# Kernel tuning notes

Hardware: AMD Instinct MI355X
Metric: run time of the kernel (lower is better)

The kernel has to match this reference:

```python
import jax, jax.numpy as jnp
import numpy as np

B, T, C, H = 2, 2048, 2048, 16
HD = C // H


def setup_inputs() -> dict:
    key = jax.random.key(0)
    ks = jax.random.split(key, 5)
    s = 0.02  # init scale for weights
    return {
        "x": jax.random.normal(ks[0], (B, T, C), jnp.float32),
        "Wq": jax.random.normal(ks[1], (C, C), jnp.float32) * s,
        "Wk": jax.random.normal(ks[2], (C, C), jnp.float32) * s,
        "Wv": jax.random.normal(ks[3], (C, C), jnp.float32) * s,
        "Wo": jax.random.normal(ks[4], (C, C), jnp.float32) * s,
        "bo": jnp.zeros((C,), jnp.float32),
    }


def _alibi_slopes(n_head):
    # power-of-2 path of _get_alibi_slopes (n_head=16 is a power of 2)
    return jnp.array([1.0 / 2 ** (i + 1) for i in range(n_head)], jnp.float32)


def reference(x, Wq, Wk, Wv, Wo, bo):
    b, t, c = x.shape
    h, hd = H, HD
    scale = 1.0 / np.sqrt(hd)
    # nn.Linear (no bias): y = x @ W.T; split heads -> (B,H,T,HD)
    q = (x @ Wq.T).reshape(b, t, h, hd).transpose(0, 2, 1, 3)
    k = (x @ Wk.T).reshape(b, t, h, hd).transpose(0, 2, 1, 3)
    v = (x @ Wv.T).reshape(b, t, h, hd).transpose(0, 2, 1, 3)
    scores = jnp.einsum("bhtd,bhsd->bhts", q, k) * scale  # (B,H,T,T)
    pos = jnp.arange(t)
    diff = pos[:, None] - pos[None, :]  # (T,T), i-j
    slopes = _alibi_slopes(h)
    bias = slopes[:, None, None] * diff.astype(jnp.float32)  # (H,T,T)
    causal = diff >= 0  # lower-triangular mask
    bias = jnp.where(causal[None, :, :], bias, -jnp.inf)
    scores = scores + bias[None]  # (B,H,T,T)
    attn = jax.nn.softmax(scores, axis=-1)  # dropout = identity (eval mode)
    out = jnp.einsum("bhts,bhsd->bhtd", attn, v)
    out = out.transpose(0, 2, 1, 3).reshape(b, t, c)
    out = out @ Wo.T + bo  # proj_dropout = identity (eval mode)
    return out, attn
```

## Files before the change

### kernel.cpp

```cpp
#include <hip/hip_runtime.h>
#include <hip/hip_bf16.h>

#define DEVINL __device__ __forceinline__

typedef __attribute__((ext_vector_type(8))) short bf16x8;
typedef __attribute__((ext_vector_type(4))) float f32x4;

DEVINL ushort f2bf(float f) {
  unsigned u = __float_as_uint(f);
  u += 0x7fffu + ((u >> 16) & 1u);
  return (ushort)(u >> 16);
}

DEVINL void gl_lds16(const void* g, void* lds) {
  __builtin_amdgcn_global_load_lds(
      (const __attribute__((address_space(1))) void*)g,
      (__attribute__((address_space(3))) void*)lds, 16, 0, 0);
}

DEVINL f32x4 mfma16(bf16x8 a, bf16x8 b, f32x4 c) {
  return __builtin_amdgcn_mfma_f32_16x16x32_bf16(a, b, c, 0, 0, 0);
}

__global__ __launch_bounds__(256) void cast_bf16_kernel(const float4* __restrict__ in,
                                                        ushort4* __restrict__ out, int n4) {
  int stride = (int)(gridDim.x * blockDim.x);
  for (int i = (int)(blockIdx.x * blockDim.x + threadIdx.x); i < n4; i += stride) {
    float4 v = in[i];
    out[i] = make_ushort4(f2bf(v.x), f2bf(v.y), f2bf(v.z), f2bf(v.w));
  }
}

template <int OUTMODE>
__global__ __launch_bounds__(256) void gemm_nt(const ushort* __restrict__ A,
                                               const ushort* __restrict__ Bm,
                                               void* __restrict__ Cout,
                                               const float* __restrict__ bias,
                                               int M, int N, int K) {
  __shared__ __align__(16) ushort Al[8192];
  __shared__ __align__(16) ushort Bl[8192];
  const int tid = (int)threadIdx.x;
  const int l = tid & 63, w = tid >> 6;
  const int wr = w >> 1, wc = w & 1;
  const int lr = l & 15, lg = l >> 4;
  const int rowT = (int)blockIdx.y * 128, colT = (int)blockIdx.x * 128;

  f32x4 acc[4][4] = {};

  for (int kt = 0; kt < K; kt += 64) {
#pragma unroll
    for (int q = 0; q < 4; ++q) {
      int s = q * 256 + tid;
      int rb = s >> 7, ks = (s >> 6) & 1, sl = s & 63;
      size_t koff = (size_t)(kt + ks * 32 + (sl >> 4) * 8);
      gl_lds16(A + (size_t)(rowT + rb * 16 + (sl & 15)) * K + koff,
               Al + (size_t)(q * 256 + (tid & 192)) * 8);
      gl_lds16(Bm + (size_t)(colT + rb * 16 + (sl & 15)) * K + koff,
               Bl + (size_t)(q * 256 + (tid & 192)) * 8);
    }
    __syncthreads();
#pragma unroll
    for (int ks = 0; ks < 2; ++ks) {
      bf16x8 af[4], bfv[4];
#pragma unroll
      for (int i = 0; i < 4; ++i) {
        af[i]  = *(const bf16x8*)(Al + (((wr * 4 + i) * 2 + ks) * 64 + l) * 8);
        bfv[i] = *(const bf16x8*)(Bl + (((wc * 4 + i) * 2 + ks) * 64 + l) * 8);
      }
#pragma unroll
      for (int i = 0; i < 4; ++i)
#pragma unroll
        for (int j = 0; j < 4; ++j)
          acc[i][j] = mfma16(af[i], bfv[j], acc[i][j]);
    }
    __syncthreads();
  }

#pragma unroll
  for (int i = 0; i < 4; ++i) {
#pragma unroll
    for (int j = 0; j < 4; ++j) {
      const int col = colT + wc * 64 + j * 16 + lr;
#pragma unroll
      for (int e = 0; e < 4; ++e) {
        const int row = rowT + wr * 64 + i * 16 + lg * 4 + e;
        float v = acc[i][j][e];
        if (OUTMODE == 0) {
          ((ushort*)Cout)[(size_t)row * N + col] = f2bf(v);
        } else if (OUTMODE == 1) {
          ((ushort*)Cout)[((size_t)((row >> 11) * 2048 + col)) * 2048 + (row & 2047)] = f2bf(v);
        } else {
          ((float*)Cout)[(size_t)row * N + col] = v + bias[col];
        }
      }
    }
  }
}

__global__ __launch_bounds__(256) void flash_kernel(const ushort* __restrict__ Qg,
                                                    const ushort* __restrict__ Kg,
                                                    const ushort* __restrict__ Vt,
                                                    ushort* __restrict__ Og,
                                                    float2* __restrict__ stats) {
  __shared__ __align__(16) ushort Kl[2][8192];
  __shared__ __align__(16) ushort Vl[2][8192];
  __shared__ __align__(16) ushort Pl[4][1024];

  const int flat = (int)(blockIdx.y * gridDim.x + blockIdx.x);
  const int swz = (flat & 7) * 64 + (flat >> 3);
  const int bx = swz & 15, bh = swz >> 4;
  const int b = bh >> 4, h = bh & 15;
  const int tid = (int)threadIdx.x, l = tid & 63, w = tid >> 6;
  const int lr = l & 15, lg = l >> 4;
  const float scale = 0.08838834764831845f;
  const float slope = exp2f(-(float)(h + 1));
  const ushort* Kbase = Kg + ((size_t)b * 2048) * 2048 + h * 128;
  const ushort* Vbase = Vt + ((size_t)b * 2048 + h * 128) * 2048;

  for (int half = 0; half < 2; ++half) {
    const int qb = (half == 0) ? 31 - bx : bx;
    const int qr0 = qb * 64 + w * 16;

    bf16x8 qf[4];
#pragma unroll
    for (int ks = 0; ks < 4; ++ks)
      qf[ks] = *(const bf16x8*)(Qg + ((size_t)b * 2048 + qr0 + lr) * 2048 + h * 128 + ks * 32 + lg * 8);

    float runmax[4], runsum[4];
    f32x4 o[8] = {};
#pragma unroll
    for (int j = 0; j < 4; ++j) { runmax[j] = -__builtin_inff(); runsum[j] = 0.f; }

    auto stage = [&](int jt, int buf) {
#pragma unroll
      for (int q = 0; q < 4; ++q) {
        const int s = q * 256 + tid;
        const int sl = s & 63;
        const int cb = s >> 8, ks = (s >> 6) & 3;
        gl_lds16(Kbase + (size_t)(jt * 64 + cb * 16 + (sl & 15)) * 2048 + ks * 32 + (sl >> 4) * 8,
                 &Kl[buf][(size_t)(q * 256 + (tid & 192)) * 8]);
        const int db = s >> 7, k2 = (s >> 6) & 1;
        gl_lds16(Vbase + (size_t)(db * 16 + (sl & 15)) * 2048 + jt * 64 + k2 * 32 + (sl >> 4) * 8,
                 &Vl[buf][(size_t)(q * 256 + (tid & 192)) * 8]);
      }
    };

    stage(qb, 0);
    __syncthreads();

    for (int jt = qb; jt >= 0; --jt) {
      const int cur = (qb - jt) & 1;
      if (jt > 0) stage(jt - 1, cur ^ 1);

      f32x4 sc[4];
#pragma unroll
      for (int cb = 0; cb < 4; ++cb) {
        f32x4 a = {};
#pragma unroll
        for (int ks = 0; ks < 4; ++ks) {
          bf16x8 kf = *(const bf16x8*)(&Kl[cur][((cb * 4 + ks) * 64 + l) * 8]);
          a = mfma16(qf[ks], kf, a);
        }
        const int kj = jt * 64 + cb * 16 + lr;
#pragma unroll
        for (int j = 0; j < 4; ++j) {
          const int qi = qr0 + lg * 4 + j;
          a[j] = (kj <= qi) ? a[j] * scale + slope * (float)(qi - kj) : -__builtin_inff();
        }
        sc[cb] = a;
      }

      float nm[4];
      bool need = false;
#pragma unroll
      for (int j = 0; j < 4; ++j) {
        float m = fmaxf(fmaxf(sc[0][j], sc[1][j]), fmaxf(sc[2][j], sc[3][j]));
#pragma unroll
        for (int d = 1; d < 16; d <<= 1) m = fmaxf(m, __shfl_xor(m, d));
        nm[j] = fmaxf(runmax[j], m);
        need = need || (nm[j] > runmax[j]);
      }
      if (__any(need)) {
#pragma unroll
        for (int j = 0; j < 4; ++j) {
          const float f = __expf(runmax[j] - nm[j]);
          runsum[j] *= f;
#pragma unroll
          for (int db = 0; db < 8; ++db) o[db][j] *= f;
          runmax[j] = nm[j];
        }
      }

#pragma unroll
      for (int cb = 0; cb < 4; ++cb) {
        const int kc = cb * 16 + lr;
#pragma unroll
        for (int j = 0; j < 4; ++j) {
          const float p = __expf(sc[cb][j] - runmax[j]);
          runsum[j] += p;
          const int l2 = (((kc & 31) >> 3) << 4) | (lg * 4 + j);
          Pl[w][((kc >> 5) * 64 + l2) * 8 + (kc & 7)] = f2bf(p);
        }
      }

      bf16x8 pf0 = *(const bf16x8*)(&Pl[w][(size_t)l * 8]);
      bf16x8 pf1 = *(const bf16x8*)(&Pl[w][(size_t)(64 + l) * 8]);
#pragma unroll
      for (int db = 0; db < 8; ++db) {
        o[db] = mfma16(pf0, *(const bf16x8*)(&Vl[cur][((db * 2 + 0) * 64 + l) * 8]), o[db]);
        o[db] = mfma16(pf1, *(const bf16x8*)(&Vl[cur][((db * 2 + 1) * 64 + l) * 8]), o[db]);
      }
      __syncthreads();
    }

#pragma unroll
    for (int j = 0; j < 4; ++j) {
      float s = runsum[j];
#pragma unroll
      for (int d = 1; d < 16; d <<= 1) s += __shfl_xor(s, d);
      const float iv = 1.0f / s;
      if (lr == 0) stats[(size_t)bh * 2048 + qr0 + lg * 4 + j] = make_float2(runmax[j], iv);
#pragma unroll
      for (int db = 0; db < 8; ++db) o[db][j] *= iv;
    }
#pragma unroll
    for (int db = 0; db < 8; ++db)
#pragma unroll
      for (int j = 0; j < 4; ++j)
        Og[((size_t)b * 2048 + qr0 + lg * 4 + j) * 2048 + h * 128 + db * 16 + lr] = f2bf(o[db][j]);
  }
}

__global__ __launch_bounds__(256) void probs_kernel(const ushort* __restrict__ Qg,
                                                    const ushort* __restrict__ Kg,
                                                    const float2* __restrict__ stats,
                                                    float* __restrict__ attn_out) {
  const int kb = (int)blockIdx.x, qb = (int)blockIdx.y, bh = (int)blockIdx.z;
  const int tid = (int)threadIdx.x;

  if (kb > qb) {
    float* base = attn_out + ((size_t)bh * 2048 + qb * 128) * 2048 + kb * 128;
    const float4 z = make_float4(0.f, 0.f, 0.f, 0.f);
#pragma unroll
    for (int it = 0; it < 16; ++it) {
      const int idx = it * 256 + tid;
      *(float4*)(base + (size_t)(idx >> 5) * 2048 + (idx & 31) * 4) = z;
    }
    return;
  }

  __shared__ __align__(16) ushort Ql[16384];
  __shared__ __align__(16) ushort Kl[16384];
  const int b = bh >> 4, h = bh & 15;
  const int l = tid & 63, w = tid >> 6;
  const int wr = w >> 1, wc = w & 1;
  const int lr = l & 15, lg = l >> 4;
  const float scale = 0.08838834764831845f;
  const float slope = exp2f(-(float)(h + 1));

#pragma unroll
  for (int q = 0; q < 8; ++q) {
    const int s = q * 256 + tid;
    const int sl = s & 63, rb = s >> 8, ks = (s >> 6) & 3;
    const size_t koff = (size_t)(h * 128 + ks * 32 + (sl >> 4) * 8);
    gl_lds16(Qg + ((size_t)b * 2048 + qb * 128 + rb * 16 + (sl & 15)) * 2048 + koff,
             Ql + (size_t)(q * 256 + (tid & 192)) * 8);
    gl_lds16(Kg + ((size_t)b * 2048 + kb * 128 + rb * 16 + (sl & 15)) * 2048 + koff,
             Kl + (size_t)(q * 256 + (tid & 192)) * 8);
  }
  __syncthreads();

  f32x4 acc[4][4] = {};
#pragma unroll
  for (int ks = 0; ks < 4; ++ks) {
    bf16x8 af[4], bfv[4];
#pragma unroll
    for (int i = 0; i < 4; ++i) {
      af[i]  = *(const bf16x8*)(Ql + (((wr * 4 + i) * 4 + ks) * 64 + l) * 8);
      bfv[i] = *(const bf16x8*)(Kl + (((wc * 4 + i) * 4 + ks) * 64 + l) * 8);
    }
#pragma unroll
    for (int i = 0; i < 4; ++i)
#pragma unroll
      for (int j = 0; j < 4; ++j)
        acc[i][j] = mfma16(af[i], bfv[j], acc[i][j]);
  }

  float2 st[4][4];
#pragma unroll
  for (int i = 0; i < 4; ++i)
#pragma unroll
    for (int e = 0; e < 4; ++e)
      st[i][e] = stats[(size_t)bh * 2048 + qb * 128 + wr * 64 + i * 16 + lg * 4 + e];

#pragma unroll
  for (int i = 0; i < 4; ++i) {
#pragma unroll
    for (int j = 0; j < 4; ++j) {
      const int kj = kb * 128 + wc * 64 + j * 16 + lr;
#pragma unroll
      for (int e = 0; e < 4; ++e) {
        const int qi = qb * 128 + wr * 64 + i * 16 + lg * 4 + e;
        const float sv = acc[i][j][e] * scale + slope * (float)(qi - kj);
        float p = __expf(sv - st[i][e].x) * st[i][e].y;
        if (kj > qi) p = 0.f;
        attn_out[((size_t)bh * 2048 + qi) * 2048 + kj] = p;
      }
    }
  }
}

extern "C" void kernel_launch(void* const* d_in, const int* in_sizes, int n_in,
                              void* d_out, int out_size, void* d_ws, size_t ws_size,
                              hipStream_t stream) {
  (void)in_sizes; (void)n_in; (void)out_size; (void)ws_size;
  const float* x  = (const float*)d_in[0];
  const float* Wq = (const float*)d_in[1];
  const float* Wk = (const float*)d_in[2];
  const float* Wv = (const float*)d_in[3];
  const float* Wo = (const float*)d_in[4];
  const float* bo = (const float*)d_in[5];

  float* outp  = (float*)d_out;
  float* attnp = outp + (size_t)4096 * 2048;

  char* ws = (char*)d_ws;
  ushort* xb  = (ushort*)(ws);
  ushort* wqb = (ushort*)(ws + (16ull << 20));
  ushort* wkb = (ushort*)(ws + (24ull << 20));
  ushort* wvb = (ushort*)(ws + (32ull << 20));
  ushort* wob = (ushort*)(ws + (40ull << 20));
  ushort* Qb  = (ushort*)(ws + (48ull << 20));
  ushort* Kb  = (ushort*)(ws + (64ull << 20));
  ushort* Vtb = (ushort*)(ws + (80ull << 20));
  ushort* Ob  = (ushort*)(ws + (96ull << 20));
  float2* stats = (float2*)(ws);

  cast_bf16_kernel<<<2048, 256, 0, stream>>>((const float4*)x,  (ushort4*)xb,  8388608 / 4);
  cast_bf16_kernel<<<1024, 256, 0, stream>>>((const float4*)Wq, (ushort4*)wqb, 4194304 / 4);
  cast_bf16_kernel<<<1024, 256, 0, stream>>>((const float4*)Wk, (ushort4*)wkb, 4194304 / 4);
  cast_bf16_kernel<<<1024, 256, 0, stream>>>((const float4*)Wv, (ushort4*)wvb, 4194304 / 4);
  cast_bf16_kernel<<<1024, 256, 0, stream>>>((const float4*)Wo, (ushort4*)wob, 4194304 / 4);

  dim3 g(16, 32);
  gemm_nt<0><<<g, 256, 0, stream>>>(xb, wqb, Qb,  nullptr, 4096, 2048, 2048);
  gemm_nt<0><<<g, 256, 0, stream>>>(xb, wkb, Kb,  nullptr, 4096, 2048, 2048);
  gemm_nt<1><<<g, 256, 0, stream>>>(xb, wvb, Vtb, nullptr, 4096, 2048, 2048);

  flash_kernel<<<dim3(16, 32), 256, 0, stream>>>(Qb, Kb, Vtb, Ob, stats);
  probs_kernel<<<dim3(16, 16, 32), 256, 0, stream>>>(Qb, Kb, stats, attnp);

  gemm_nt<2><<<g, 256, 0, stream>>>(Ob, wob, outp, bo, 4096, 2048, 2048);
}
```

Measured before the change: 568.6 us.

## Fuse QKV projections into one GEMM, double-buffer GEMM LDS, add setprio

The three Q/K/V projection GEMMs are merged into one launch over a concatenated weight matrix (N=6144), with the epilogue routing each column segment to Q, K or transposed V. The GEMM gains double-buffered LDS staging so the next K-tile loads while the current one is computed, plus an XCD-aware block-index swizzle. The flash kernel wraps its MFMA sections in s_setprio to favour matrix issue. Together these aim to cut launch count, raise occupancy across the device and hide load latency, at the cost of doubled GEMM LDS use, which may lower occupancy.

Measured after the change: 575.2 us. About the same (+1.2%).

```diff
diff --git a/kernel.cpp b/kernel.cpp
--- a/kernel.cpp
+++ b/kernel.cpp
@@ -31,41 +31,55 @@
   }
 }
 
-template <int OUTMODE>
+template <int MODE>
 __global__ __launch_bounds__(256) void gemm_nt(const ushort* __restrict__ A,
                                                const ushort* __restrict__ Bm,
-                                               void* __restrict__ Cout,
+                                               ushort* __restrict__ Qo,
+                                               ushort* __restrict__ Ko,
+                                               ushort* __restrict__ Vo,
+                                               float* __restrict__ Fo,
                                                const float* __restrict__ bias,
                                                int M, int N, int K) {
-  __shared__ __align__(16) ushort Al[8192];
-  __shared__ __align__(16) ushort Bl[8192];
+  __shared__ __align__(16) ushort Al[2][8192];
+  __shared__ __align__(16) ushort Bl[2][8192];
   const int tid = (int)threadIdx.x;
   const int l = tid & 63, w = tid >> 6;
   const int wr = w >> 1, wc = w & 1;
   const int lr = l & 15, lg = l >> 4;
-  const int rowT = (int)blockIdx.y * 128, colT = (int)blockIdx.x * 128;
+
+  const int nwg = (int)(gridDim.x * gridDim.y);
+  const int flat = (int)(blockIdx.y * gridDim.x + blockIdx.x);
+  const int swz = (flat & 7) * (nwg >> 3) + (flat >> 3);
+  const int bx = swz % (int)gridDim.x, by = swz / (int)gridDim.x;
+  const int rowT = by * 128, colT = bx * 128;
 
   f32x4 acc[4][4] = {};
 
-  for (int kt = 0; kt < K; kt += 64) {
+  auto stage = [&](int kt, int buf) {
 #pragma unroll
     for (int q = 0; q < 4; ++q) {
       int s = q * 256 + tid;
       int rb = s >> 7, ks = (s >> 6) & 1, sl = s & 63;
       size_t koff = (size_t)(kt + ks * 32 + (sl >> 4) * 8);
       gl_lds16(A + (size_t)(rowT + rb * 16 + (sl & 15)) * K + koff,
-               Al + (size_t)(q * 256 + (tid & 192)) * 8);
+               &Al[buf][(size_t)(q * 256 + (tid & 192)) * 8]);
       gl_lds16(Bm + (size_t)(colT + rb * 16 + (sl & 15)) * K + koff,
-               Bl + (size_t)(q * 256 + (tid & 192)) * 8);
-    }
-    __syncthreads();
+               &Bl[buf][(size_t)(q * 256 + (tid & 192)) * 8]);
+    }
+  };
+
+  stage(0, 0);
+  __syncthreads();
+  int cur = 0;
+  for (int kt = 0; kt < K; kt += 64) {
+    if (kt + 64 < K) stage(kt + 64, cur ^ 1);
 #pragma unroll
     for (int ks = 0; ks < 2; ++ks) {
       bf16x8 af[4], bfv[4];
 #pragma unroll
       for (int i = 0; i < 4; ++i) {
-        af[i]  = *(const bf16x8*)(Al + (((wr * 4 + i) * 2 + ks) * 64 + l) * 8);
-        bfv[i] = *(const bf16x8*)(Bl + (((wc * 4 + i) * 2 + ks) * 64 + l) * 8);
+        af[i]  = *(const bf16x8*)(&Al[cur][(((wr * 4 + i) * 2 + ks) * 64 + l) * 8]);
+        bfv[i] = *(const bf16x8*)(&Bl[cur][(((wc * 4 + i) * 2 + ks) * 64 + l) * 8]);
       }
 #pragma unroll
       for (int i = 0; i < 4; ++i)
@@ -74,8 +88,10 @@
           acc[i][j] = mfma16(af[i], bfv[j], acc[i][j]);
     }
     __syncthreads();
-  }
-
+    cur ^= 1;
+  }
+
+  const int seg = colT >> 11;
 #pragma unroll
   for (int i = 0; i < 4; ++i) {
 #pragma unroll
@@ -85,12 +101,13 @@
       for (int e = 0; e < 4; ++e) {
         const int row = rowT + wr * 64 + i * 16 + lg * 4 + e;
         float v = acc[i][j][e];
-        if (OUTMODE == 0) {
-          ((ushort*)Cout)[(size_t)row * N + col] = f2bf(v);
-        } else if (OUTMODE == 1) {
-          ((ushort*)Cout)[((size_t)((row >> 11) * 2048 + col)) * 2048 + (row & 2047)] = f2bf(v);
+        if (MODE == 3) {
+          const int c = col & 2047;
+          if (seg == 0)      Qo[(size_t)row * 2048 + c] = f2bf(v);
+          else if (seg == 1) Ko[(size_t)row * 2048 + c] = f2bf(v);
+          else               Vo[((size_t)((row >> 11) * 2048 + c)) * 2048 + (row & 2047)] = f2bf(v);
         } else {
-          ((float*)Cout)[(size_t)row * N + col] = v + bias[col];
+          Fo[(size_t)row * 2048 + col] = v + bias[col];
         }
       }
     }
@@ -153,6 +170,7 @@
       if (jt > 0) stage(jt - 1, cur ^ 1);
 
       f32x4 sc[4];
+      __builtin_amdgcn_s_setprio(1);
 #pragma unroll
       for (int cb = 0; cb < 4; ++cb) {
         f32x4 a = {};
@@ -161,13 +179,17 @@
           bf16x8 kf = *(const bf16x8*)(&Kl[cur][((cb * 4 + ks) * 64 + l) * 8]);
           a = mfma16(qf[ks], kf, a);
         }
+        sc[cb] = a;
+      }
+      __builtin_amdgcn_s_setprio(0);
+#pragma unroll
+      for (int cb = 0; cb < 4; ++cb) {
         const int kj = jt * 64 + cb * 16 + lr;
 #pragma unroll
         for (int j = 0; j < 4; ++j) {
           const int qi = qr0 + lg * 4 + j;
-          a[j] = (kj <= qi) ? a[j] * scale + slope * (float)(qi - kj) : -__builtin_inff();
-        }
-        sc[cb] = a;
+          sc[cb][j] = (kj <= qi) ? sc[cb][j] * scale + slope * (float)(qi - kj) : -__builtin_inff();
+        }
       }
 
       float nm[4];
@@ -205,11 +227,13 @@
 
       bf16x8 pf0 = *(const bf16x8*)(&Pl[w][(size_t)l * 8]);
       bf16x8 pf1 = *(const bf16x8*)(&Pl[w][(size_t)(64 + l) * 8]);
+      __builtin_amdgcn_s_setprio(1);
 #pragma unroll
       for (int db = 0; db < 8; ++db) {
         o[db] = mfma16(pf0, *(const bf16x8*)(&Vl[cur][((db * 2 + 0) * 64 + l) * 8]), o[db]);
         o[db] = mfma16(pf1, *(const bf16x8*)(&Vl[cur][((db * 2 + 1) * 64 + l) * 8]), o[db]);
       }
+      __builtin_amdgcn_s_setprio(0);
       __syncthreads();
     }
 
@@ -325,30 +349,27 @@
   float* attnp = outp + (size_t)4096 * 2048;
 
   char* ws = (char*)d_ws;
-  ushort* xb  = (ushort*)(ws);
-  ushort* wqb = (ushort*)(ws + (16ull << 20));
-  ushort* wkb = (ushort*)(ws + (24ull << 20));
-  ushort* wvb = (ushort*)(ws + (32ull << 20));
-  ushort* wob = (ushort*)(ws + (40ull << 20));
-  ushort* Qb  = (ushort*)(ws + (48ull << 20));
-  ushort* Kb  = (ushort*)(ws + (64ull << 20));
-  ushort* Vtb = (ushort*)(ws + (80ull << 20));
-  ushort* Ob  = (ushort*)(ws + (96ull << 20));
+  ushort* xb   = (ushort*)(ws);
+  ushort* wqkv = (ushort*)(ws + (16ull << 20));
+  ushort* wob  = (ushort*)(ws + (40ull << 20));
+  ushort* Qb   = (ushort*)(ws + (48ull << 20));
+  ushort* Kb   = (ushort*)(ws + (64ull << 20));
+  ushort* Vtb  = (ushort*)(ws + (80ull << 20));
+  ushort* Ob   = (ushort*)(ws + (96ull << 20));
   float2* stats = (float2*)(ws);
 
-  cast_bf16_kernel<<<2048, 256, 0, stream>>>((const float4*)x,  (ushort4*)xb,  8388608 / 4);
-  cast_bf16_kernel<<<1024, 256, 0, stream>>>((const float4*)Wq, (ushort4*)wqb, 4194304 / 4);
-  cast_bf16_kernel<<<1024, 256, 0, stream>>>((const float4*)Wk, (ushort4*)wkb, 4194304 / 4);
-  cast_bf16_kernel<<<1024, 256, 0, stream>>>((const float4*)Wv, (ushort4*)wvb, 4194304 / 4);
+  cast_bf16_kernel<<<2048, 256, 0, stream>>>((const float4*)x,  (ushort4*)xb, 8388608 / 4);
+  cast_bf16_kernel<<<1024, 256, 0, stream>>>((const float4*)Wq, (ushort4*)(wqkv),               4194304 / 4);
+  cast_bf16_kernel<<<1024, 256, 0, stream>>>((const float4*)Wk, (ushort4*)(wqkv + 4194304),     4194304 / 4);
+  cast_bf16_kernel<<<1024, 256, 0, stream>>>((const float4*)Wv, (ushort4*)(wqkv + 2 * 4194304), 4194304 / 4);
   cast_bf16_kernel<<<1024, 256, 0, stream>>>((const float4*)Wo, (ushort4*)wob, 4194304 / 4);
 
-  dim3 g(16, 32);
-  gemm_nt<0><<<g, 256, 0, stream>>>(xb, wqb, Qb,  nullptr, 4096, 2048, 2048);
-  gemm_nt<0><<<g, 256, 0, stream>>>(xb, wkb, Kb,  nullptr, 4096, 2048, 2048);
-  gemm_nt<1><<<g, 256, 0, stream>>>(xb, wvb, Vtb, nullptr, 4096, 2048, 2048);
+  gemm_nt<3><<<dim3(48, 32), 256, 0, stream>>>(xb, wqkv, Qb, Kb, Vtb, nullptr, nullptr,
+                                               4096, 6144, 2048);
 
   flash_kernel<<<dim3(16, 32), 256, 0, stream>>>(Qb, Kb, Vtb, Ob, stats);
   probs_kernel<<<dim3(16, 16, 32), 256, 0, stream>>>(Qb, Kb, stats, attnp);
 
-  gemm_nt<2><<<g, 256, 0, stream>>>(Ob, wob, outp, bo, 4096, 2048, 2048);
-}
+  gemm_nt<2><<<dim3(16, 32), 256, 0, stream>>>(Ob, wob, nullptr, nullptr, nullptr, outp, bo,
+                                               4096, 2048, 2048);
+}
```
